# Kernel optimization log

Measured on AMD Instinct MI355X. Metric: run time of the kernel, lower is better.

## Reference

```python
import jax, jax.numpy as jnp
import numpy as np

N_NODES = 100000
DIM_IN = 128
DIM_H = 64
LATENT = 64
N_EDGES = 1200000


def setup_inputs() -> dict:
    key = jax.random.key(0)
    ks = jax.random.split(key, 8)
    x = jax.random.normal(ks[0], (N_NODES, DIM_IN), dtype=jnp.float32)
    edge_index = jax.random.randint(ks[1], (2, N_EDGES), 0, N_NODES, dtype=jnp.int32)
    batch = jnp.zeros((N_NODES,), dtype=jnp.int32)
    s_in = 1.0 / np.sqrt(DIM_IN)
    s_h = 1.0 / np.sqrt(DIM_H)
    gcn_w = jax.random.uniform(ks[2], (DIM_IN, DIM_H), jnp.float32, -s_in, s_in)
    gcn_b = jnp.zeros((DIM_H,), dtype=jnp.float32)
    w1 = jax.random.uniform(ks[3], (DIM_H, LATENT), jnp.float32, -s_h, s_h)
    b1 = jax.random.uniform(ks[4], (LATENT,), jnp.float32, -s_h, s_h)
    s_l = 1.0 / np.sqrt(LATENT)
    w3 = jax.random.uniform(ks[5], (LATENT, LATENT), jnp.float32, -s_l, s_l)
    b3 = jax.random.uniform(ks[6], (LATENT,), jnp.float32, -s_l, s_l)
    return {"x": x, "edge_index": edge_index, "batch": batch,
            "gcn_w": gcn_w, "gcn_b": gcn_b, "w1": w1, "b1": b1, "w3": w3, "b3": b3}


def _gcn_conv(x, edge_index, W, b):
    n = x.shape[0]
    loop = jnp.arange(n, dtype=edge_index.dtype)
    src = jnp.concatenate([edge_index[0], loop])
    dst = jnp.concatenate([edge_index[1], loop])
    deg = jax.ops.segment_sum(jnp.ones_like(dst, dtype=x.dtype), dst, num_segments=n)
    dinv = jnp.where(deg > 0, jax.lax.rsqrt(deg), 0.0)
    norm = dinv[src] * dinv[dst]                      # [E+N]
    h = x @ W                                          # [N, dim_h]
    msg = h[src] * norm[:, None]                       # gather + scale
    out = jax.ops.segment_sum(msg, dst, num_segments=n)  # scatter-add
    return out + b


def reference(x, edge_index, batch, gcn_w, gcn_b, w1, b1, w3, b3):
    g1 = _gcn_conv(x, edge_index, gcn_w, gcn_b)
    l1 = g1 @ w1 + b1
    l3 = l1 @ w3 + b3
    # mu/sigma/z/kl in the original are side effects not returned; output is l3
    return l3
```

## Files before the change

### kernel.cpp

```cpp
#include <hip/hip_runtime.h>
#include <hip/hip_bf16.h>

#define N_NODES 100000
#define N_EDGES 1200000
#define NBK 256
#define NPB 391
#define CAPB 5376
#define EPB 4096
#define BIN_GRID 293

typedef __attribute__((ext_vector_type(8))) short bf16x8;
typedef __attribute__((ext_vector_type(4))) float f32x4;

__global__ __launch_bounds__(256) void k_w1(const float* __restrict__ w1,
                                            const float* __restrict__ w3,
                                            const float* __restrict__ gcn_b,
                                            const float* __restrict__ b1,
                                            float* __restrict__ tmp,
                                            float* __restrict__ tb) {
    const int i = blockIdx.x * 256 + threadIdx.x;
    const int r = i >> 6, c = i & 63;
    float a = 0.f;
#pragma unroll 8
    for (int k = 0; k < 64; ++k) a = fmaf(w1[r * 64 + k], w3[k * 64 + c], a);
    tmp[i] = a;
    if (blockIdx.x == 0 && threadIdx.x < 64) {
        const int t = threadIdx.x;
        float s = b1[t];
        for (int k = 0; k < 64; ++k) s = fmaf(gcn_b[k], w1[k * 64 + t], s);
        tb[t] = s;
    }
}

__global__ __launch_bounds__(256) void k_w2(const float* __restrict__ gcn_w,
                                            const float* __restrict__ tmp,
                                            const float* __restrict__ tb,
                                            const float* __restrict__ w3,
                                            const float* __restrict__ b3,
                                            short* __restrict__ WcB,
                                            float* __restrict__ bc) {
    const int i = blockIdx.x * 256 + threadIdx.x;
    const int r = i >> 6, c = i & 63;
    float a = 0.f;
#pragma unroll 8
    for (int k = 0; k < 64; ++k) a = fmaf(gcn_w[r * 64 + k], tmp[k * 64 + c], a);
    const int kt = r >> 5, kr = r & 31, g = kr >> 3, e = kr & 7;
    const int ct = c >> 4, cl = c & 15, lane = g * 16 + cl;
    WcB[(((kt * 4 + ct) * 64) + lane) * 8 + e] =
        __builtin_bit_cast(short, __float2bfloat16(a));
    if (blockIdx.x == 0 && threadIdx.x < 64) {
        const int t = threadIdx.x;
        float s = b3[t];
        for (int k = 0; k < 64; ++k) s = fmaf(tb[k], w3[k * 64 + t], s);
        bc[t] = s;
    }
}

__global__ __launch_bounds__(256) void k_bin(const int* __restrict__ ei,
                                             int* __restrict__ bcnt,
                                             int* __restrict__ binned) {
    __shared__ int hist[NBK], base[NBK], cur[NBK];
    const int t = threadIdx.x;
    const int e0 = blockIdx.x * EPB;
    for (int i = t; i < NBK; i += 256) hist[i] = 0;
    __syncthreads();
    for (int j = t; j < EPB; j += 256) {
        const int e = e0 + j;
        if (e < N_EDGES) atomicAdd(&hist[ei[N_EDGES + e] / NPB], 1);
    }
    __syncthreads();
    for (int i = t; i < NBK; i += 256) {
        const int h = hist[i];
        base[i] = h ? atomicAdd(&bcnt[i], h) : 0;
        cur[i] = 0;
    }
    __syncthreads();
    for (int j = t; j < EPB; j += 256) {
        const int e = e0 + j;
        if (e < N_EDGES) {
            const int s = ei[e];
            const int d = ei[N_EDGES + e];
            const int b = d / NPB;
            const int dl = d - b * NPB;
            const int p = base[b] + atomicAdd(&cur[b], 1);
            if (p < CAPB) binned[b * CAPB + p] = s | (dl << 17);
        }
    }
}

__global__ __launch_bounds__(256) void k_csr(const int* __restrict__ bcnt,
                                             const int* __restrict__ binned,
                                             int* __restrict__ csr,
                                             int* __restrict__ rowptr,
                                             int* __restrict__ degA,
                                             float* __restrict__ dinv) {
    __shared__ int stage[CAPB];
    __shared__ int sdeg[NPB], sloc[NPB], scur[NPB];
    const int b = blockIdx.x, t = threadIdx.x;
    const int m = min(bcnt[b], CAPB);
    for (int i = t; i < NPB; i += 256) { sdeg[i] = 0; scur[i] = 0; }
    __syncthreads();
    for (int j = t; j < m; j += 256) {
        const int pk = binned[b * CAPB + j];
        stage[j] = pk;
        atomicAdd(&sdeg[pk >> 17], 1);
    }
    __syncthreads();
    if (t < 64) {
        int run = 0;
#pragma unroll
        for (int c0 = 0; c0 < NPB; c0 += 64) {
            const int idx = c0 + t;
            const int v = (idx < NPB) ? sdeg[idx] : 0;
            int inc = v;
#pragma unroll
            for (int o = 1; o < 64; o <<= 1) {
                const int u = __shfl_up(inc, o);
                if (t >= o) inc += u;
            }
            if (idx < NPB) sloc[idx] = run + inc - v;
            run += __shfl(inc, 63);
        }
    }
    __syncthreads();
    for (int i = t; i < NPB; i += 256) {
        const int node = b * NPB + i;
        if (node < N_NODES) {
            const int v = sdeg[i];
            rowptr[node] = b * CAPB + sloc[i];
            degA[node] = v;
            dinv[node] = rsqrtf((float)(v + 1));
        }
    }
    for (int j = t; j < m; j += 256) {
        const int pk = stage[j];
        const int dl = pk >> 17;
        const int p = atomicAdd(&scur[dl], 1);
        csr[b * CAPB + sloc[dl] + p] = pk & 0x1FFFF;
    }
}

__global__ __launch_bounds__(256) void k_xw(const float* __restrict__ x,
                                            const short* __restrict__ WcB,
                                            __hip_bfloat16* __restrict__ hs) {
    const int t = threadIdx.x, w = t >> 6, lane = t & 63;
    const int cl = lane & 15, g = lane >> 4;
    bf16x8 bfrag[16];
#pragma unroll
    for (int f = 0; f < 16; ++f) bfrag[f] = ((const bf16x8*)WcB)[f * 64 + lane];

    const int ntiles = N_NODES / 16;
    const int nw = gridDim.x * 4;
    for (int tile = blockIdx.x * 4 + w; tile < ntiles; tile += nw) {
        const int node0 = tile * 16;
        const float* xrow = x + (size_t)(node0 + cl) * 128 + g * 8;
        f32x4 xa[4][2];
#pragma unroll
        for (int kt = 0; kt < 4; ++kt) {
            xa[kt][0] = *(const f32x4*)(xrow + kt * 32);
            xa[kt][1] = *(const f32x4*)(xrow + kt * 32 + 4);
        }
        f32x4 acc[4];
#pragma unroll
        for (int ct = 0; ct < 4; ++ct) acc[ct] = (f32x4){0.f, 0.f, 0.f, 0.f};
#pragma unroll
        for (int kt = 0; kt < 4; ++kt) {
            bf16x8 af;
#pragma unroll
            for (int j = 0; j < 4; ++j) {
                af[j]     = __builtin_bit_cast(short, __float2bfloat16(xa[kt][0][j]));
                af[j + 4] = __builtin_bit_cast(short, __float2bfloat16(xa[kt][1][j]));
            }
#pragma unroll
            for (int ct = 0; ct < 4; ++ct)
                acc[ct] = __builtin_amdgcn_mfma_f32_16x16x32_bf16(
                    af, bfrag[kt * 4 + ct], acc[ct], 0, 0, 0);
        }
#pragma unroll
        for (int ct = 0; ct < 4; ++ct)
#pragma unroll
            for (int j = 0; j < 4; ++j)
                hs[(size_t)(node0 + g * 4 + j) * 64 + ct * 16 + cl] =
                    __float2bfloat16(acc[ct][j]);
    }
}

__global__ __launch_bounds__(256) void k_gather(const int* __restrict__ rowptr,
                                                const int* __restrict__ degA,
                                                const int* __restrict__ csr,
                                                const __hip_bfloat16* __restrict__ hs,
                                                const float* __restrict__ dinv,
                                                const float* __restrict__ bc,
                                                float* __restrict__ out) {
    const int t = threadIdx.x, wave = t >> 6, lane = t & 63;
    const int node = blockIdx.x * 4 + wave;
    if (node >= N_NODES) return;
    const int deg = degA[node];
    const int base = rowptr[node];
    const float dvn = dinv[node];
    const int cl = lane & 15, g = lane >> 4;
    const int cc = cl * 4;

    f32x4 acc = (f32x4){0.f, 0.f, 0.f, 0.f};
    for (int j0 = 0; j0 < deg; j0 += 64) {
        const int rem = min(deg - j0, 64);
        int s_l = 0;
        float dv_l = 0.f;
        if (lane < rem) {
            s_l = csr[base + j0 + lane];
            dv_l = dinv[s_l];
        }
        for (int i0 = 0; i0 < rem; i0 += 16) {
#pragma unroll
            for (int u = 0; u < 4; ++u) {
                const int jj = i0 + u * 4 + g;
                const int sj = __shfl(s_l, jj);
                const float dj = __shfl(dv_l, jj);
                if (jj < rem) {
                    const ushort4 hv =
                        *(const ushort4*)(hs + (size_t)sj * 64 + cc);
                    acc[0] = fmaf(__bfloat162float(__builtin_bit_cast(__hip_bfloat16, hv.x)), dj, acc[0]);
                    acc[1] = fmaf(__bfloat162float(__builtin_bit_cast(__hip_bfloat16, hv.y)), dj, acc[1]);
                    acc[2] = fmaf(__bfloat162float(__builtin_bit_cast(__hip_bfloat16, hv.z)), dj, acc[2]);
                    acc[3] = fmaf(__bfloat162float(__builtin_bit_cast(__hip_bfloat16, hv.w)), dj, acc[3]);
                }
            }
        }
    }
#pragma unroll
    for (int k = 0; k < 4; ++k) {
        acc[k] += __shfl_xor(acc[k], 16);
        acc[k] += __shfl_xor(acc[k], 32);
    }
    const ushort4 hvs = *(const ushort4*)(hs + (size_t)node * 64 + cc);
    const float4 bc4 = *(const float4*)(bc + cc);
    float4 res;
    res.x = fmaf(fmaf(__bfloat162float(__builtin_bit_cast(__hip_bfloat16, hvs.x)), dvn, acc[0]), dvn, bc4.x);
    res.y = fmaf(fmaf(__bfloat162float(__builtin_bit_cast(__hip_bfloat16, hvs.y)), dvn, acc[1]), dvn, bc4.y);
    res.z = fmaf(fmaf(__bfloat162float(__builtin_bit_cast(__hip_bfloat16, hvs.z)), dvn, acc[2]), dvn, bc4.z);
    res.w = fmaf(fmaf(__bfloat162float(__builtin_bit_cast(__hip_bfloat16, hvs.w)), dvn, acc[3]), dvn, bc4.w);
    if (g == 0) *(float4*)(out + (size_t)node * 64 + cc) = res;
}

extern "C" void kernel_launch(void* const* d_in, const int* in_sizes, int n_in,
                              void* d_out, int out_size, void* d_ws, size_t ws_size,
                              hipStream_t stream) {
    const float* x     = (const float*)d_in[0];
    const int*   ei    = (const int*)d_in[1];
    const float* gcn_w = (const float*)d_in[3];
    const float* gcn_b = (const float*)d_in[4];
    const float* w1    = (const float*)d_in[5];
    const float* b1    = (const float*)d_in[6];
    const float* w3    = (const float*)d_in[7];
    const float* b3    = (const float*)d_in[8];
    float* out = (float*)d_out;

    char* ws = (char*)d_ws;
    int*            bcnt   = (int*)(ws);
    short*          WcB    = (short*)(ws + 1024);
    float*          bc     = (float*)(ws + 17408);
    float*          tmp    = (float*)(ws + 17664);
    float*          tb     = (float*)(ws + 34048);
    float*          dinv   = (float*)(ws + 34304);
    int*            rowptr = (int*)(ws + 434304);
    int*            degA   = (int*)(ws + 834304);
    __hip_bfloat16* hs     = (__hip_bfloat16*)(ws + 1234304);
    int*            binned = (int*)(ws + 14034304);
    int*            csr    = (int*)(ws + 19539328);

    hipMemsetAsync(bcnt, 0, NBK * sizeof(int), stream);
    k_w1<<<16, 256, 0, stream>>>(w1, w3, gcn_b, b1, tmp, tb);
    k_w2<<<32, 256, 0, stream>>>(gcn_w, tmp, tb, w3, b3, WcB, bc);
    k_bin<<<BIN_GRID, 256, 0, stream>>>(ei, bcnt, binned);
    k_csr<<<NBK, 256, 0, stream>>>(bcnt, binned, csr, rowptr, degA, dinv);
    k_xw<<<1024, 256, 0, stream>>>(x, WcB, hs);
    k_gather<<<(N_NODES + 3) / 4, 256, 0, stream>>>(rowptr, degA, csr, hs, dinv, bc, out);
}
```

Baseline: 119.1 us.

## Quantize node features to int8 and fuse X·W into binning kernel

Merges the edge-binning kernel and the X·W MFMA projection into one launch, with the block range split between the two jobs so they run concurrently. The projected features are stored as per-row scaled 8-bit values (offset by 128) instead of bf16, and the weight fragment layout is permuted so each lane packs four adjacent columns into one 32-bit word. The gather kernel reads one int per neighbour, dequantizes by folding scale times dinv into one coefficient, and subtracts the 128 offset at the end. This halves the bytes read in the random-access gather and removes a launch, at the cost of lower numeric precision that may exceed tolerance.

```diff
diff --git a/kernel.cpp b/kernel.cpp
--- a/kernel.cpp
+++ b/kernel.cpp
@@ -7,7 +7,9 @@
 #define NPB 391
 #define CAPB 5376
 #define EPB 4096
-#define BIN_GRID 293
+#define BIN_BLKS 293
+#define XW_BLKS 1280
+#define FUSED_GRID (BIN_BLKS + XW_BLKS)
 
 typedef __attribute__((ext_vector_type(8))) short bf16x8;
 typedef __attribute__((ext_vector_type(4))) float f32x4;
@@ -45,7 +47,7 @@
 #pragma unroll 8
     for (int k = 0; k < 64; ++k) a = fmaf(gcn_w[r * 64 + k], tmp[k * 64 + c], a);
     const int kt = r >> 5, kr = r & 31, g = kr >> 3, e = kr & 7;
-    const int ct = c >> 4, cl = c & 15, lane = g * 16 + cl;
+    const int ct = c & 3, cl = c >> 2, lane = g * 16 + cl;
     WcB[(((kt * 4 + ct) * 64) + lane) * 8 + e] =
         __builtin_bit_cast(short, __float2bfloat16(a));
     if (blockIdx.x == 0 && threadIdx.x < 64) {
@@ -56,34 +58,100 @@
     }
 }
 
-__global__ __launch_bounds__(256) void k_bin(const int* __restrict__ ei,
-                                             int* __restrict__ bcnt,
-                                             int* __restrict__ binned) {
-    __shared__ int hist[NBK], base[NBK], cur[NBK];
-    const int t = threadIdx.x;
-    const int e0 = blockIdx.x * EPB;
-    for (int i = t; i < NBK; i += 256) hist[i] = 0;
-    __syncthreads();
-    for (int j = t; j < EPB; j += 256) {
-        const int e = e0 + j;
-        if (e < N_EDGES) atomicAdd(&hist[ei[N_EDGES + e] / NPB], 1);
-    }
-    __syncthreads();
-    for (int i = t; i < NBK; i += 256) {
-        const int h = hist[i];
-        base[i] = h ? atomicAdd(&bcnt[i], h) : 0;
-        cur[i] = 0;
-    }
-    __syncthreads();
-    for (int j = t; j < EPB; j += 256) {
-        const int e = e0 + j;
-        if (e < N_EDGES) {
-            const int s = ei[e];
-            const int d = ei[N_EDGES + e];
-            const int b = d / NPB;
-            const int dl = d - b * NPB;
-            const int p = base[b] + atomicAdd(&cur[b], 1);
-            if (p < CAPB) binned[b * CAPB + p] = s | (dl << 17);
+__global__ __launch_bounds__(256) void k_fused(const int* __restrict__ ei,
+                                               int* __restrict__ bcnt,
+                                               int* __restrict__ binned,
+                                               const float* __restrict__ x,
+                                               const short* __restrict__ WcB,
+                                               unsigned char* __restrict__ hsq,
+                                               float* __restrict__ hscale) {
+    const int b = blockIdx.x;
+    if (b < BIN_BLKS) {
+        __shared__ int hist[NBK], base[NBK], cur[NBK];
+        const int t = threadIdx.x;
+        const int e0 = b * EPB;
+        for (int i = t; i < NBK; i += 256) hist[i] = 0;
+        __syncthreads();
+        for (int j = t; j < EPB; j += 256) {
+            const int e = e0 + j;
+            if (e < N_EDGES) atomicAdd(&hist[ei[N_EDGES + e] / NPB], 1);
+        }
+        __syncthreads();
+        for (int i = t; i < NBK; i += 256) {
+            const int h = hist[i];
+            base[i] = h ? atomicAdd(&bcnt[i], h) : 0;
+            cur[i] = 0;
+        }
+        __syncthreads();
+        for (int j = t; j < EPB; j += 256) {
+            const int e = e0 + j;
+            if (e < N_EDGES) {
+                const int s = ei[e];
+                const int d = ei[N_EDGES + e];
+                const int bk = d / NPB;
+                const int dl = d - bk * NPB;
+                const int p = base[bk] + atomicAdd(&cur[bk], 1);
+                if (p < CAPB) binned[bk * CAPB + p] = s | (dl << 17);
+            }
+        }
+    } else {
+        const int t = threadIdx.x, w = t >> 6, lane = t & 63;
+        const int cl = lane & 15, g = lane >> 4;
+        bf16x8 bfrag[16];
+#pragma unroll
+        for (int f = 0; f < 16; ++f) bfrag[f] = ((const bf16x8*)WcB)[f * 64 + lane];
+
+        const int ntiles = N_NODES / 16;
+        const int nw = XW_BLKS * 4;
+        for (int tile = (b - BIN_BLKS) * 4 + w; tile < ntiles; tile += nw) {
+            const int node0 = tile * 16;
+            const float* xrow = x + (size_t)(node0 + cl) * 128 + g * 8;
+            f32x4 xa[4][2];
+#pragma unroll
+            for (int kt = 0; kt < 4; ++kt) {
+                xa[kt][0] = *(const f32x4*)(xrow + kt * 32);
+                xa[kt][1] = *(const f32x4*)(xrow + kt * 32 + 4);
+            }
+            f32x4 acc[4];
+#pragma unroll
+            for (int ct = 0; ct < 4; ++ct) acc[ct] = (f32x4){0.f, 0.f, 0.f, 0.f};
+#pragma unroll
+            for (int kt = 0; kt < 4; ++kt) {
+                bf16x8 af;
+#pragma unroll
+                for (int j = 0; j < 4; ++j) {
+                    af[j]     = __builtin_bit_cast(short, __float2bfloat16(xa[kt][0][j]));
+                    af[j + 4] = __builtin_bit_cast(short, __float2bfloat16(xa[kt][1][j]));
+                }
+#pragma unroll
+                for (int ct = 0; ct < 4; ++ct)
+                    acc[ct] = __builtin_amdgcn_mfma_f32_16x16x32_bf16(
+                        af, bfrag[kt * 4 + ct], acc[ct], 0, 0, 0);
+            }
+            float mx[4];
+#pragma unroll
+            for (int j = 0; j < 4; ++j) {
+                mx[j] = fmaxf(fmaxf(fabsf(acc[0][j]), fabsf(acc[1][j])),
+                              fmaxf(fabsf(acc[2][j]), fabsf(acc[3][j])));
+            }
+#pragma unroll
+            for (int m = 1; m < 16; m <<= 1)
+#pragma unroll
+                for (int j = 0; j < 4; ++j)
+                    mx[j] = fmaxf(mx[j], __shfl_xor(mx[j], m));
+#pragma unroll
+            for (int j = 0; j < 4; ++j) {
+                const float sc = fmaxf(mx[j], 1e-20f) * (1.f / 127.f);
+                const float inv = 127.f / fmaxf(mx[j], 1e-20f);
+                unsigned int pk = 0;
+#pragma unroll
+                for (int ct = 0; ct < 4; ++ct) {
+                    const int v = (int)rintf(acc[ct][j] * inv) + 128;
+                    pk |= (unsigned int)v << (8 * ct);
+                }
+                *(unsigned int*)(hsq + (size_t)(node0 + g * 4 + j) * 64 + cl * 4) = pk;
+                if (cl == j) hscale[node0 + g * 4 + j] = sc;
+            }
         }
     }
 }
@@ -140,55 +208,11 @@
     }
 }
 
-__global__ __launch_bounds__(256) void k_xw(const float* __restrict__ x,
-                                            const short* __restrict__ WcB,
-                                            __hip_bfloat16* __restrict__ hs) {
-    const int t = threadIdx.x, w = t >> 6, lane = t & 63;
-    const int cl = lane & 15, g = lane >> 4;
-    bf16x8 bfrag[16];
-#pragma unroll
-    for (int f = 0; f < 16; ++f) bfrag[f] = ((const bf16x8*)WcB)[f * 64 + lane];
-
-    const int ntiles = N_NODES / 16;
-    const int nw = gridDim.x * 4;
-    for (int tile = blockIdx.x * 4 + w; tile < ntiles; tile += nw) {
-        const int node0 = tile * 16;
-        const float* xrow = x + (size_t)(node0 + cl) * 128 + g * 8;
-        f32x4 xa[4][2];
-#pragma unroll
-        for (int kt = 0; kt < 4; ++kt) {
-            xa[kt][0] = *(const f32x4*)(xrow + kt * 32);
-            xa[kt][1] = *(const f32x4*)(xrow + kt * 32 + 4);
-        }
-        f32x4 acc[4];
-#pragma unroll
-        for (int ct = 0; ct < 4; ++ct) acc[ct] = (f32x4){0.f, 0.f, 0.f, 0.f};
-#pragma unroll
-        for (int kt = 0; kt < 4; ++kt) {
-            bf16x8 af;
-#pragma unroll
-            for (int j = 0; j < 4; ++j) {
-                af[j]     = __builtin_bit_cast(short, __float2bfloat16(xa[kt][0][j]));
-                af[j + 4] = __builtin_bit_cast(short, __float2bfloat16(xa[kt][1][j]));
-            }
-#pragma unroll
-            for (int ct = 0; ct < 4; ++ct)
-                acc[ct] = __builtin_amdgcn_mfma_f32_16x16x32_bf16(
-                    af, bfrag[kt * 4 + ct], acc[ct], 0, 0, 0);
-        }
-#pragma unroll
-        for (int ct = 0; ct < 4; ++ct)
-#pragma unroll
-            for (int j = 0; j < 4; ++j)
-                hs[(size_t)(node0 + g * 4 + j) * 64 + ct * 16 + cl] =
-                    __float2bfloat16(acc[ct][j]);
-    }
-}
-
 __global__ __launch_bounds__(256) void k_gather(const int* __restrict__ rowptr,
                                                 const int* __restrict__ degA,
                                                 const int* __restrict__ csr,
-                                                const __hip_bfloat16* __restrict__ hs,
+                                                const unsigned char* __restrict__ hsq,
+                                                const float* __restrict__ hscale,
                                                 const float* __restrict__ dinv,
                                                 const float* __restrict__ bc,
                                                 float* __restrict__ out) {
@@ -202,43 +226,47 @@
     const int cc = cl * 4;
 
     f32x4 acc = (f32x4){0.f, 0.f, 0.f, 0.f};
+    float T = 0.f;
     for (int j0 = 0; j0 < deg; j0 += 64) {
         const int rem = min(deg - j0, 64);
         int s_l = 0;
-        float dv_l = 0.f;
+        float c_l = 0.f;
         if (lane < rem) {
             s_l = csr[base + j0 + lane];
-            dv_l = dinv[s_l];
+            c_l = dinv[s_l] * hscale[s_l];
         }
         for (int i0 = 0; i0 < rem; i0 += 16) {
 #pragma unroll
             for (int u = 0; u < 4; ++u) {
                 const int jj = i0 + u * 4 + g;
                 const int sj = __shfl(s_l, jj);
-                const float dj = __shfl(dv_l, jj);
+                const float cj = __shfl(c_l, jj);
                 if (jj < rem) {
-                    const ushort4 hv =
-                        *(const ushort4*)(hs + (size_t)sj * 64 + cc);
-                    acc[0] = fmaf(__bfloat162float(__builtin_bit_cast(__hip_bfloat16, hv.x)), dj, acc[0]);
-                    acc[1] = fmaf(__bfloat162float(__builtin_bit_cast(__hip_bfloat16, hv.y)), dj, acc[1]);
-                    acc[2] = fmaf(__bfloat162float(__builtin_bit_cast(__hip_bfloat16, hv.z)), dj, acc[2]);
-                    acc[3] = fmaf(__bfloat162float(__builtin_bit_cast(__hip_bfloat16, hv.w)), dj, acc[3]);
+                    const unsigned int q =
+                        *(const unsigned int*)(hsq + (size_t)sj * 64 + cc);
+                    acc[0] = fmaf((float)(q & 0xFFu), cj, acc[0]);
+                    acc[1] = fmaf((float)((q >> 8) & 0xFFu), cj, acc[1]);
+                    acc[2] = fmaf((float)((q >> 16) & 0xFFu), cj, acc[2]);
+                    acc[3] = fmaf((float)(q >> 24), cj, acc[3]);
+                    T += cj;
                 }
             }
         }
     }
 #pragma unroll
     for (int k = 0; k < 4; ++k) {
+        acc[k] = fmaf(-128.f, T, acc[k]);
         acc[k] += __shfl_xor(acc[k], 16);
         acc[k] += __shfl_xor(acc[k], 32);
     }
-    const ushort4 hvs = *(const ushort4*)(hs + (size_t)node * 64 + cc);
+    const unsigned int qs = *(const unsigned int*)(hsq + (size_t)node * 64 + cc);
+    const float cs = dvn * hscale[node];
     const float4 bc4 = *(const float4*)(bc + cc);
     float4 res;
-    res.x = fmaf(fmaf(__bfloat162float(__builtin_bit_cast(__hip_bfloat16, hvs.x)), dvn, acc[0]), dvn, bc4.x);
-    res.y = fmaf(fmaf(__bfloat162float(__builtin_bit_cast(__hip_bfloat16, hvs.y)), dvn, acc[1]), dvn, bc4.y);
-    res.z = fmaf(fmaf(__bfloat162float(__builtin_bit_cast(__hip_bfloat16, hvs.z)), dvn, acc[2]), dvn, bc4.z);
-    res.w = fmaf(fmaf(__bfloat162float(__builtin_bit_cast(__hip_bfloat16, hvs.w)), dvn, acc[3]), dvn, bc4.w);
+    res.x = fmaf(fmaf(((float)(qs & 0xFFu)) - 128.f, cs, acc[0]), dvn, bc4.x);
+    res.y = fmaf(fmaf(((float)((qs >> 8) & 0xFFu)) - 128.f, cs, acc[1]), dvn, bc4.y);
+    res.z = fmaf(fmaf(((float)((qs >> 16) & 0xFFu)) - 128.f, cs, acc[2]), dvn, bc4.z);
+    res.w = fmaf(fmaf(((float)(qs >> 24)) - 128.f, cs, acc[3]), dvn, bc4.w);
     if (g == 0) *(float4*)(out + (size_t)node * 64 + cc) = res;
 }
 
@@ -256,23 +284,24 @@
     float* out = (float*)d_out;
 
     char* ws = (char*)d_ws;
-    int*            bcnt   = (int*)(ws);
-    short*          WcB    = (short*)(ws + 1024);
-    float*          bc     = (float*)(ws + 17408);
-    float*          tmp    = (float*)(ws + 17664);
-    float*          tb     = (float*)(ws + 34048);
-    float*          dinv   = (float*)(ws + 34304);
-    int*            rowptr = (int*)(ws + 434304);
-    int*            degA   = (int*)(ws + 834304);
-    __hip_bfloat16* hs     = (__hip_bfloat16*)(ws + 1234304);
-    int*            binned = (int*)(ws + 14034304);
-    int*            csr    = (int*)(ws + 19539328);
+    int*           bcnt   = (int*)(ws);
+    short*         WcB    = (short*)(ws + 1024);
+    float*         bc     = (float*)(ws + 17408);
+    float*         tmp    = (float*)(ws + 17664);
+    float*         tb     = (float*)(ws + 34048);
+    float*         dinv   = (float*)(ws + 34304);
+    int*           rowptr = (int*)(ws + 434304);
+    int*           degA   = (int*)(ws + 834304);
+    float*         hscale = (float*)(ws + 1234304);
+    unsigned char* hsq    = (unsigned char*)(ws + 1634304);
+    int*           binned = (int*)(ws + 8034304);
+    int*           csr    = (int*)(ws + 13539328);
 
     hipMemsetAsync(bcnt, 0, NBK * sizeof(int), stream);
     k_w1<<<16, 256, 0, stream>>>(w1, w3, gcn_b, b1, tmp, tb);
     k_w2<<<32, 256, 0, stream>>>(gcn_w, tmp, tb, w3, b3, WcB, bc);
-    k_bin<<<BIN_GRID, 256, 0, stream>>>(ei, bcnt, binned);
+    k_fused<<<FUSED_GRID, 256, 0, stream>>>(ei, bcnt, binned, x, WcB, hsq, hscale);
     k_csr<<<NBK, 256, 0, stream>>>(bcnt, binned, csr, rowptr, degA, dinv);
-    k_xw<<<1024, 256, 0, stream>>>(x, WcB, hs);
-    k_gather<<<(N_NODES + 3) / 4, 256, 0, stream>>>(rowptr, degA, csr, hs, dinv, bc, out);
-}
+    k_gather<<<(N_NODES + 3) / 4, 256, 0, stream>>>(rowptr, degA, csr, hsq, hscale,
+                                                    dinv, bc, out);
+}
```

Result: faster. 109.0 us (-8.5%).
